# Optimization experiments

Measured on AMD Instinct MI355X. Metric: run time of the kernel, lower is better.

The kernel has to match this reference:

```python
import jax, jax.numpy as jnp
import numpy as np

NEG = -9e8

def _leaky(x):
    return jax.nn.leaky_relu(x, 0.01)

def _gru(x, h, wih, whh, bih, bhh):
    # torch.nn.GRUCell math
    gi = x @ wih.T + bih
    gh = h @ whh.T + bhh
    ir, iz, inn = jnp.split(gi, 3, axis=-1)
    hr, hz, hn = jnp.split(gh, 3, axis=-1)
    r = jax.nn.sigmoid(ir + hr)
    z = jax.nn.sigmoid(iz + hz)
    n = jnp.tanh(inn + r * hn)
    return (1.0 - z) * n + z * h

def _gather(feat, idx):
    # feat [B,S,F], idx [B,S,K] -> [B,S,K,F]; -1 wraps to last row, masked later (same as torch)
    return jax.vmap(lambda f, i: f[i])(feat, idx)

def setup_inputs() -> dict:
    key = jax.random.key(0)
    ks = jax.random.split(key, 32)
    B, S, K, F_in, E, R = 32, 512, 21, 26, 256, 3
    amino_list = jax.random.uniform(ks[0], (B, S, F_in), dtype=jnp.float32)
    idx = jax.random.randint(ks[1], (B, S, K), 0, S, dtype=jnp.int32)
    pad = jax.random.uniform(ks[2], (B, S, K)) < 0.3
    amino_degree_list = jnp.where(pad, jnp.int32(-1), idx)
    # variable sequence lengths for mask
    lens = jax.random.randint(ks[3], (B,), S // 2, S + 1)
    amino_mask = (jnp.arange(S)[None, :] < lens[:, None]).astype(jnp.float32)
    s = 0.05
    d = dict(
        amino_list=amino_list,
        amino_degree_list=amino_degree_list,
        amino_mask=amino_mask,
        emb_W=jax.random.normal(ks[4], (E, F_in)) * s,
        emb_b=jax.random.normal(ks[5], (E,)) * s,
        neigh_W=jax.random.normal(ks[6], (E, F_in)) * s,
        neigh_b=jax.random.normal(ks[7], (E,)) * s,
        align_W=jax.random.normal(ks[8], (R, 1, 2 * E)) * s,
        align_b=jax.random.normal(ks[9], (R, 1)) * s,
        attend_W=jax.random.normal(ks[10], (R, E, E)) * s,
        attend_b=jax.random.normal(ks[11], (R, E)) * s,
        gru_wih=jax.random.normal(ks[12], (R, 3 * E, E)) * s,
        gru_whh=jax.random.normal(ks[13], (R, 3 * E, E)) * s,
        gru_bih=jax.random.normal(ks[14], (R, 3 * E)) * s,
        gru_bhh=jax.random.normal(ks[15], (R, 3 * E)) * s,
        seq_align_W=jax.random.normal(ks[16], (1, 2 * E)) * s,
        seq_align_b=jax.random.normal(ks[17], (1,)) * s,
        seq_attend_W=jax.random.normal(ks[18], (E, E)) * s,
        seq_attend_b=jax.random.normal(ks[19], (E,)) * s,
        sgru_wih=jax.random.normal(ks[20], (3 * E, E)) * s,
        sgru_whh=jax.random.normal(ks[21], (3 * E, E)) * s,
        sgru_bih=jax.random.normal(ks[22], (3 * E,)) * s,
        sgru_bhh=jax.random.normal(ks[23], (3 * E,)) * s,
    )
    return d

RADIUS = 3
T_STEPS = 2

def reference(amino_list, amino_degree_list, amino_mask,
              emb_W, emb_b, neigh_W, neigh_b,
              align_W, align_b, attend_W, attend_b,
              gru_wih, gru_whh, gru_bih, gru_bhh,
              seq_align_W, seq_align_b, seq_attend_W, seq_attend_b,
              sgru_wih, sgru_whh, sgru_bih, sgru_bhh):
    B, S, _ = amino_list.shape
    E = emb_W.shape[0]
    K = amino_degree_list.shape[-1]

    mask3 = amino_mask[:, :, None]                       # [B,S,1]
    amino_feature = _leaky(amino_list @ emb_W.T + emb_b)  # [B,S,E]

    attend_mask = (amino_degree_list != -1).astype(jnp.float32)[..., None]   # [B,S,K,1]
    softmax_mask = jnp.where(amino_degree_list == -1, NEG, 0.0)[..., None]   # [B,S,K,1]

    # first radius step: neighbors from raw one-hot features via neighbor_fc
    neighbor = _gather(amino_list, amino_degree_list)                 # [B,S,K,F_in]
    neighbor_feature = _leaky(neighbor @ neigh_W.T + neigh_b)         # [B,S,K,E]

    h = amino_feature.reshape(B * S, E)
    activated = None
    for d in range(RADIUS):
        if d == 0:
            nbr = neighbor_feature
            cur = amino_feature
        else:
            nbr = _gather(activated, amino_degree_list)               # [B,S,K,E]
            cur = activated
        cur_exp = jnp.broadcast_to(cur[:, :, None, :], (B, S, K, E))
        feat_align = jnp.concatenate([cur_exp, nbr], axis=-1)         # [B,S,K,2E]
        score = _leaky(feat_align @ align_W[d].T + align_b[d]) + softmax_mask
        attw = jax.nn.softmax(score, axis=-2) * attend_mask           # [B,S,K,1]
        nbr_t = nbr @ attend_W[d].T + attend_b[d]                     # [B,S,K,E]
        context = jax.nn.elu(jnp.sum(attw * nbr_t, axis=-2))          # [B,S,E]
        h = _gru(context.reshape(B * S, E), h, gru_wih[d], gru_whh[d], gru_bih[d], gru_bhh[d])
        activated = jax.nn.relu(h.reshape(B, S, E))

    seq_feature = jnp.sum(activated * mask3, axis=-2)                 # [B,E]
    act_mol = jax.nn.relu(seq_feature)
    seq_softmax_mask = jnp.where(mask3 == 0.0, NEG, 0.0)              # [B,S,1]

    act_seq = act_mol
    for _ in range(T_STEPS):
        mol_exp = jnp.broadcast_to(act_mol[:, None, :], (B, S, E))
        sa = jnp.concatenate([mol_exp, activated], axis=-1)           # [B,S,2E]
        score = _leaky(sa @ seq_align_W.T + seq_align_b) + seq_softmax_mask
        w = jax.nn.softmax(score, axis=-2) * mask3                    # [B,S,1]
        feat_t = activated @ seq_attend_W.T + seq_attend_b            # [B,S,E]
        seq_context = jax.nn.elu(jnp.sum(w * feat_t, axis=-2))        # [B,E]
        seq_feature = _gru(seq_context, seq_feature, sgru_wih, sgru_whh, sgru_bih, sgru_bhh)
        act_seq = jax.nn.relu(seq_feature)
    return act_seq
```

## Files before the change

### kernel.cpp

```cpp
#include <hip/hip_runtime.h>
#include <hip/hip_bf16.h>
#include <math.h>


#define NEGC (-9.0e8f)

typedef __attribute__((ext_vector_type(8))) short bf16x8;
typedef __attribute__((ext_vector_type(4))) float f32x4;

__device__ __forceinline__ ushort f2bf(float x) {
    union { float f; unsigned u; } v; v.f = x;
    unsigned r = v.u + 0x7FFF + ((v.u >> 16) & 1);
    return (ushort)(r >> 16);
}
__device__ __forceinline__ float bf2f(ushort u) {
    union { unsigned u; float f; } v; v.u = ((unsigned)u) << 16;
    return v.f;
}
__device__ __forceinline__ float sigm_fast(float x) {
    return 1.f / (1.f + __expf(-x));
}
__device__ __forceinline__ float tanh_fast(float x) {
    return 1.f - 2.f / (__expf(2.f * x) + 1.f);
}
__device__ __forceinline__ float elu_fast(float x) {
    return x > 0.f ? x : (__expf(x) - 1.f);
}
__device__ __forceinline__ bf16x8 relu_bf8(bf16x8 v) {
    bf16x8 r;
#pragma unroll
    for (int i = 0; i < 8; ++i)
        r[i] = (v[i] & (short)0x8000) ? (short)0 : v[i];
    return r;
}

typedef const __attribute__((address_space(1))) void gvoid_t;
typedef __attribute__((address_space(3))) void lvoid_t;

__global__ __launch_bounds__(256) void cvt3_kernel(
    const float* __restrict__ s0, ushort* __restrict__ d0, int n0,
    const float* __restrict__ s1, ushort* __restrict__ d1, int n1,
    const float* __restrict__ s2, ushort* __restrict__ d2, int n2)
{
    int i = blockIdx.x * 256 + threadIdx.x;
    const float* s; ushort* dst; int l;
    if (i < n0) { s = s0; dst = d0; l = i; }
    else if (i < n0 + n1) { s = s1; dst = d1; l = i - n0; }
    else if (i < n0 + n1 + n2) { s = s2; dst = d2; l = i - n0 - n1; }
    else return;
    float4 v = *reinterpret_cast<const float4*>(s + (size_t)l * 4);
    ushort4 o; o.x = f2bf(v.x); o.y = f2bf(v.y); o.z = f2bf(v.z); o.w = f2bf(v.w);
    *reinterpret_cast<ushort4*>(dst + (size_t)l * 4) = o;
}

template<bool RELUA>
__global__ __launch_bounds__(256) void gemm_dual_kernel(
    const ushort* __restrict__ A0, const ushort* __restrict__ W0,
    const float* __restrict__ b0, ushort* __restrict__ C0, int n0t,
    int K,
    const float* __restrict__ dw1, const float* __restrict__ dw2,
    float* __restrict__ dout1, float* __restrict__ dout2)
{
    __shared__ __align__(16) short As[128 * 32];
    __shared__ __align__(16) short Bs[128 * 32];
    int nwg = gridDim.x;
    int q = nwg >> 3;
    int flat = blockIdx.x;
    int sw = (flat & 7) * q + (flat >> 3);
    int bmi = sw / n0t, bni = sw - bmi * n0t;
    const ushort* A = A0; const ushort* W = W0; const float* bias = b0;
    ushort* C = C0; int N = n0t << 7; int bn = bni << 7;
    int bm = bmi << 7;

    int tid = threadIdx.x;
    int lane = tid & 63;
    int w = tid >> 6;
    int wr = w >> 1, wc = w & 1;
    bool dots = (dout1 != nullptr) && (bni == 0);

    f32x4 acc[4][4];
#pragma unroll
    for (int m = 0; m < 4; ++m)
#pragma unroll
        for (int n = 0; n < 4; ++n) acc[m][n] = (f32x4){0.f, 0.f, 0.f, 0.f};
    float p1 = 0.f, p2 = 0.f;

    for (int k0 = 0; k0 < K; k0 += 32) {
#pragma unroll
        for (int i = 0; i < 2; ++i) {
            int e = w * 1024 + i * 512 + lane * 8;
            int r = e >> 5, c = e & 31;
            const ushort* ga = A + (size_t)(bm + r) * K + (k0 + c);
            const ushort* gw = W + (size_t)(bn + r) * K + (k0 + c);
            __builtin_amdgcn_global_load_lds((gvoid_t*)ga, (lvoid_t*)&As[w * 1024 + i * 512], 16, 0, 0);
            __builtin_amdgcn_global_load_lds((gvoid_t*)gw, (lvoid_t*)&Bs[w * 1024 + i * 512], 16, 0, 0);
        }
        __syncthreads();
        bf16x8 af[4], bw[4];
        int ra = wr * 64 + (lane & 15);
        int rb = wc * 64 + (lane & 15);
        int kc = (lane >> 4) * 8;
#pragma unroll
        for (int m = 0; m < 4; ++m) {
            af[m] = *reinterpret_cast<const bf16x8*>(&As[(ra + m * 16) * 32 + kc]);
            if (RELUA) af[m] = relu_bf8(af[m]);
        }
#pragma unroll
        for (int n = 0; n < 4; ++n)
            bw[n] = *reinterpret_cast<const bf16x8*>(&Bs[(rb + n * 16) * 32 + kc]);
#pragma unroll
        for (int m = 0; m < 4; ++m)
#pragma unroll
            for (int n = 0; n < 4; ++n)
                acc[m][n] = __builtin_amdgcn_mfma_f32_16x16x32_bf16(af[m], bw[n], acc[m][n], 0, 0, 0);
        if (dots) {
            int drow = tid >> 1, kh = (tid & 1) << 4;
            const short* ar = &As[drow * 32 + kh];
#pragma unroll
            for (int c = 0; c < 16; ++c) {
                float av = bf2f((ushort)ar[c]);
                if (RELUA) av = fmaxf(av, 0.f);
                p1 = fmaf(av, dw1[k0 + kh + c], p1);
                p2 = fmaf(av, dw2[k0 + kh + c], p2);
            }
        }
        __syncthreads();
    }

    if (dots) {
        p1 += __shfl_xor(p1, 1);
        p2 += __shfl_xor(p2, 1);
        if ((tid & 1) == 0) {
            dout1[bm + (tid >> 1)] = p1;
            dout2[bm + (tid >> 1)] = p2;
        }
    }

    int cr0 = bm + wr * 64 + ((lane >> 4) * 4);
    int cc0 = bn + wc * 64 + (lane & 15);
#pragma unroll
    for (int n = 0; n < 4; ++n) {
        int col = cc0 + n * 16;
        float bv = bias[col];
#pragma unroll
        for (int m = 0; m < 4; ++m) {
            int row0 = cr0 + m * 16;
#pragma unroll
            for (int j = 0; j < 4; ++j) {
                float v = acc[m][n][j] + bv;
                C[(size_t)(row0 + j) * N + col] = f2bf(v);
            }
        }
    }
}

template<bool TAIL>
__global__ __launch_bounds__(256) void gru_fused_kernel(
    const ushort* __restrict__ ctx, const ushort* __restrict__ wih,
    const float* __restrict__ bih, const ushort* __restrict__ whh,
    const float* __restrict__ bhh,
    const ushort* __restrict__ h_in, ushort* __restrict__ h_out,
    const float* __restrict__ mask, float* __restrict__ pool_part,
    const float* __restrict__ dsw, float* __restrict__ scor_part, int BS)
{
    __shared__ __align__(16) short lds[16384];
    int flat = blockIdx.x;
    int sw = (flat & 7) * 128 + (flat >> 3);
    int bmi = sw >> 2, ct = sw & 3;
    int bm = bmi << 6;
    int tid = threadIdx.x;
    int lane = tid & 63;
    int w = tid >> 6;
    int wr = w >> 1, wc = w & 1;

    f32x4 acc[6][2][2];
#pragma unroll
    for (int qq = 0; qq < 6; ++qq)
#pragma unroll
        for (int m = 0; m < 2; ++m)
#pragma unroll
            for (int n = 0; n < 2; ++n) acc[qq][m][n] = (f32x4){0.f, 0.f, 0.f, 0.f};

    int srow = tid >> 2, scol = (tid & 3) << 3;
    int ldst = (tid & 0xC0) * 8;
    for (int k0 = 0; k0 < 256; k0 += 32) {
        {
            const ushort* s0 = ctx  + (size_t)(bm + srow) * 256 + k0 + scol;
            const ushort* s1 = h_in + (size_t)(bm + srow) * 256 + k0 + scol;
            __builtin_amdgcn_global_load_lds((gvoid_t*)s0, (lvoid_t*)&lds[ldst], 16, 0, 0);
            __builtin_amdgcn_global_load_lds((gvoid_t*)s1, (lvoid_t*)&lds[2048 + ldst], 16, 0, 0);
#pragma unroll
            for (int qq = 0; qq < 6; ++qq) {
                const ushort* wb = (qq < 3) ? wih : whh;
                int slice = (qq < 3) ? qq : qq - 3;
                const ushort* sv = wb + (size_t)(slice * 256 + ct * 64 + srow) * 256 + k0 + scol;
                __builtin_amdgcn_global_load_lds((gvoid_t*)sv,
                    (lvoid_t*)&lds[(2 + qq) * 2048 + ldst], 16, 0, 0);
            }
        }
        __syncthreads();
        int rl = lane & 15;
        int kc = (lane >> 4) * 8;
        bf16x8 a_c[2], a_h[2];
#pragma unroll
        for (int m = 0; m < 2; ++m) {
            a_c[m] = *reinterpret_cast<const bf16x8*>(&lds[(wr * 32 + m * 16 + rl) * 32 + kc]);
            a_h[m] = *reinterpret_cast<const bf16x8*>(&lds[2048 + (wr * 32 + m * 16 + rl) * 32 + kc]);
        }
#pragma unroll
        for (int qq = 0; qq < 6; ++qq) {
            bf16x8 bw[2];
#pragma unroll
            for (int n = 0; n < 2; ++n)
                bw[n] = *reinterpret_cast<const bf16x8*>(
                    &lds[(2 + qq) * 2048 + (wc * 32 + n * 16 + rl) * 32 + kc]);
#pragma unroll
            for (int m = 0; m < 2; ++m)
#pragma unroll
                for (int n = 0; n < 2; ++n)
                    acc[qq][m][n] = __builtin_amdgcn_mfma_f32_16x16x32_bf16(
                        (qq < 3) ? a_c[m] : a_h[m], bw[n], acc[qq][m][n], 0, 0, 0);
        }
        __syncthreads();
    }

    int rl = lane & 15;
    int r0 = (lane >> 4) * 4;
    float mv[2][4];
    float dswv[2];
    if (TAIL) {
        int b_ = bm >> 9;
        int sbase = bm & 511;
#pragma unroll
        for (int m = 0; m < 2; ++m)
#pragma unroll
            for (int j = 0; j < 4; ++j)
                mv[m][j] = mask[b_ * 512 + sbase + wr * 32 + m * 16 + r0 + j];
#pragma unroll
        for (int n = 0; n < 2; ++n)
            dswv[n] = dsw[ct * 64 + wc * 32 + n * 16 + rl];
    }
    float pm[2] = {0.f, 0.f};
    float ps[2][4] = {{0.f, 0.f, 0.f, 0.f}, {0.f, 0.f, 0.f, 0.f}};

#pragma unroll
    for (int n = 0; n < 2; ++n) {
        int col = ct * 64 + wc * 32 + n * 16 + rl;
        float bir = bih[col], biz = bih[256 + col], bin = bih[512 + col];
        float bhr = bhh[col], bhz = bhh[256 + col], bhn = bhh[512 + col];
#pragma unroll
        for (int m = 0; m < 2; ++m) {
            int row0 = bm + wr * 32 + m * 16 + r0;
#pragma unroll
            for (int j = 0; j < 4; ++j) {
                size_t idx = (size_t)(row0 + j) * 256 + col;
                float r = sigm_fast(acc[0][m][n][j] + bir + acc[3][m][n][j] + bhr);
                float z = sigm_fast(acc[1][m][n][j] + biz + acc[4][m][n][j] + bhz);
                float nn = tanh_fast(acc[2][m][n][j] + bin + r * (acc[5][m][n][j] + bhn));
                float hold = bf2f(h_in[idx]);
                float hh = (1.f - z) * nn + z * hold;
                ushort hb = f2bf(hh);
                h_out[idx] = hb;
                if (TAIL) {
                    float a = fmaxf(bf2f(hb), 0.f);
                    pm[n] = fmaf(a, mv[m][j], pm[n]);
                    ps[m][j] = fmaf(a, dswv[n], ps[m][j]);
                }
            }
        }
    }

    if (TAIL) {
#pragma unroll
        for (int n = 0; n < 2; ++n) {
            float p = pm[n];
            p += __shfl_xor(p, 16);
            p += __shfl_xor(p, 32);
            if (lane < 16) {
                int b_ = bm >> 9;
                int sc = ((bm & 511) >> 5) + wr;
                int col = ct * 64 + wc * 32 + n * 16 + rl;
                pool_part[((size_t)b_ * 16 + sc) * 256 + col] = p;
            }
        }
#pragma unroll
        for (int m = 0; m < 2; ++m)
#pragma unroll
            for (int j = 0; j < 4; ++j) {
                float p = ps[m][j];
                p += __shfl_xor(p, 1);
                p += __shfl_xor(p, 2);
                p += __shfl_xor(p, 4);
                p += __shfl_xor(p, 8);
                if (rl == 0) {
                    int row = bm + wr * 32 + m * 16 + r0 + j;
                    scor_part[(size_t)(ct * 2 + wc) * BS + row] = p;
                }
            }
    }
}

__global__ __launch_bounds__(256) void embed_kernel(
    const float* __restrict__ amino, const float* __restrict__ embW,
    const float* __restrict__ embB, const float* __restrict__ neighW,
    const float* __restrict__ neighB, const float* __restrict__ alignW,
    ushort* __restrict__ h_bf, ushort* __restrict__ nf_bf,
    float* __restrict__ ca, float* __restrict__ cb)
{
    const int FIN = 26, FPAD = 28, ROWS = 64;
    __shared__ __align__(16) float xs[ROWS][FPAD];
    __shared__ float red1[ROWS][4];
    __shared__ float red2[ROWS][4];
    int tid = threadIdx.x;
    int lane = tid & 63, wv = tid >> 6;
    float wE[FPAD], wN[FPAD];
#pragma unroll
    for (int f = 0; f < FIN; ++f) {
        wE[f] = embW[tid * FIN + f];
        wN[f] = neighW[tid * FIN + f];
    }
    wE[26] = wE[27] = wN[26] = wN[27] = 0.f;
    float b1 = embB[tid], b2 = neighB[tid];
    float w1t = alignW[tid], w2t = alignW[256 + tid];
    int row0 = blockIdx.x * ROWS;
    for (int idx = tid; idx < ROWS * FPAD; idx += 256) {
        int r = idx / FPAD, f = idx - r * FPAD;
        xs[r][f] = (f < FIN) ? amino[(size_t)(row0 + r) * FIN + f] : 0.f;
    }
    __syncthreads();
    for (int r = 0; r < ROWS; ++r) {
        const float4* x4 = reinterpret_cast<const float4*>(xs[r]);
        float a = b1, c = b2;
#pragma unroll
        for (int q = 0; q < 7; ++q) {
            float4 x = x4[q];
            a = fmaf(x.x, wE[4 * q], a);     c = fmaf(x.x, wN[4 * q], c);
            a = fmaf(x.y, wE[4 * q + 1], a); c = fmaf(x.y, wN[4 * q + 1], c);
            a = fmaf(x.z, wE[4 * q + 2], a); c = fmaf(x.z, wN[4 * q + 2], c);
            a = fmaf(x.w, wE[4 * q + 3], a); c = fmaf(x.w, wN[4 * q + 3], c);
        }
        a = a > 0.f ? a : 0.01f * a;
        c = c > 0.f ? c : 0.01f * c;
        size_t idx = (size_t)(row0 + r) * 256 + tid;
        h_bf[idx] = f2bf(a);
        nf_bf[idx] = f2bf(c);
        float p1 = a * w1t, p2 = c * w2t;
#pragma unroll
        for (int off = 32; off > 0; off >>= 1) {
            p1 += __shfl_down(p1, off);
            p2 += __shfl_down(p2, off);
        }
        if (lane == 0) { red1[r][wv] = p1; red2[r][wv] = p2; }
    }
    __syncthreads();
    if (tid < ROWS)
        ca[row0 + tid] = red1[tid][0] + red1[tid][1] + red1[tid][2] + red1[tid][3];
    else if (tid < 2 * ROWS) {
        int r = tid - ROWS;
        cb[row0 + r] = red2[r][0] + red2[r][1] + red2[r][2] + red2[r][3];
    }
}

__global__ __launch_bounds__(256) void attn_kernel(
    const int* __restrict__ deg, const float* __restrict__ ca,
    const float* __restrict__ cbrow, const ushort* __restrict__ act_t,
    const float* __restrict__ alignB, int d,
    ushort* __restrict__ context_bf, int S)
{
    const int KNB = 21;
    int raw = blockIdx.x;
    int bid = (raw & 7) * 512 + (raw >> 3);
    int bs0 = bid * 4;
    int b = bs0 >> 9;
    int tid = threadIdx.x;
    int wv = tid >> 6, lane = tid & 63;
    int bs = bs0 + wv;
    __shared__ float ss[4][KNB];
    __shared__ int   sj[4][KNB];
    if (lane < KNB) {
        int j = deg[bs * KNB + lane];
        float cbv = (j >= 0) ? cbrow[b * S + j] : 0.f;
        float sc = ca[bs] + cbv + alignB[d];
        sc = sc > 0.f ? sc : 0.01f * sc;
        if (j < 0) sc += NEGC;
        sj[wv][lane] = j;
        ss[wv][lane] = sc;
    }
    __syncthreads();
    float mx = -3.4e38f;
#pragma unroll
    for (int k = 0; k < KNB; ++k) mx = fmaxf(mx, ss[wv][k]);
    float se[KNB];
    int js[KNB];
    float sum = 0.f;
#pragma unroll
    for (int k = 0; k < KNB; ++k) {
        int j = sj[wv][k];
        float e = __expf(ss[wv][k] - mx);
        sum += e;
        se[k] = (j >= 0) ? e : 0.f;
        js[k] = (j >= 0) ? j : 0;
    }
    float inv = 1.f / sum;
    const ushort* base = act_t + (size_t)b * S * 256 + lane * 4;
    float a0 = 0.f, a1 = 0.f, a2 = 0.f, a3 = 0.f;
#pragma unroll
    for (int k = 0; k < KNB; ++k) {
        ushort4 v = *reinterpret_cast<const ushort4*>(base + (size_t)js[k] * 256);
        float wk = se[k];
        a0 = fmaf(wk, bf2f(v.x), a0);
        a1 = fmaf(wk, bf2f(v.y), a1);
        a2 = fmaf(wk, bf2f(v.z), a2);
        a3 = fmaf(wk, bf2f(v.w), a3);
    }
    ushort4 o;
    o.x = f2bf(elu_fast(a0 * inv));
    o.y = f2bf(elu_fast(a1 * inv));
    o.z = f2bf(elu_fast(a2 * inv));
    o.w = f2bf(elu_fast(a3 * inv));
    *reinterpret_cast<ushort4*>(&context_bf[(size_t)bs * 256 + lane * 4]) = o;
}

__global__ __launch_bounds__(256) void seqpool_sm_kernel(
    const float* __restrict__ partial, const float* __restrict__ saW,
    const float* __restrict__ scor_part, const float* __restrict__ sab,
    const float* __restrict__ mask,
    float* __restrict__ seqfeat, float* __restrict__ wout,
    float* __restrict__ wsumb, int NC, int S, int BS)
{
    int b = blockIdx.x, tid = threadIdx.x;
    int lane = tid & 63, wv = tid >> 6;
    __shared__ float red[4];
    __shared__ float sw[512];
    __shared__ float r1[4], r2[4], r3[4];
    __shared__ float smd;
    float acc = 0.f;
    for (int c = 0; c < NC; ++c)
        acc += partial[((size_t)b * NC + c) * 256 + tid];
    seqfeat[b * 256 + tid] = acc;
    float am = fmaxf(acc, 0.f);
    float p = am * saW[tid];
#pragma unroll
    for (int off = 32; off > 0; off >>= 1) p += __shfl_down(p, off);
    if (lane == 0) red[wv] = p;
    __syncthreads();
    if (tid == 0) smd = red[0] + red[1] + red[2] + red[3];
    __syncthreads();
    float md = smd, sb = sab[0];
    float lm = -3.4e38f;
    for (int s = tid; s < S; s += 256) {
        int row = b * S + s;
        float praw = 0.f;
#pragma unroll
        for (int sl = 0; sl < 8; ++sl) praw += scor_part[(size_t)sl * BS + row];
        float sc = md + praw + sb;
        sc = sc > 0.f ? sc : 0.01f * sc;
        if (mask[row] == 0.f) sc += NEGC;
        sw[s] = sc;
        lm = fmaxf(lm, sc);
    }
#pragma unroll
    for (int off = 32; off > 0; off >>= 1) lm = fmaxf(lm, __shfl_down(lm, off));
    if (lane == 0) r1[wv] = lm;
    __syncthreads();
    float mx = fmaxf(fmaxf(r1[0], r1[1]), fmaxf(r1[2], r1[3]));
    float ls = 0.f, ms = 0.f;
    for (int s = tid; s < S; s += 256) {
        float e = __expf(sw[s] - mx);
        float em = e * mask[b * S + s];
        sw[s] = em;
        ls += e;
        ms += em;
    }
#pragma unroll
    for (int off = 32; off > 0; off >>= 1) {
        ls += __shfl_down(ls, off);
        ms += __shfl_down(ms, off);
    }
    if (lane == 0) { r2[wv] = ls; r3[wv] = ms; }
    __syncthreads();
    float inv = 1.f / (r2[0] + r2[1] + r2[2] + r2[3]);
    if (tid == 0) wsumb[b] = (r3[0] + r3[1] + r3[2] + r3[3]) * inv;
    for (int s = tid; s < S; s += 256)
        wout[b * S + s] = sw[s] * inv;
}

__global__ __launch_bounds__(256) void wpool_kernel(
    const float* __restrict__ w, const ushort* __restrict__ h,
    float* __restrict__ vpart, int S, int CH)
{
    int bc = blockIdx.x;
    int NC = S / CH;
    int b = bc / NC, c = bc - b * NC;
    int tid = threadIdx.x;
    int s0 = c * CH;
    const ushort* ab = h + ((size_t)b * S + s0) * 256;
    const float* wb = w + b * S + s0;
    float acc = 0.f;
    for (int s = 0; s < CH; ++s)
        acc = fmaf(wb[s], fmaxf(bf2f(ab[(size_t)s * 256 + tid]), 0.f), acc);
    vpart[(size_t)bc * 256 + tid] = acc;
}

__global__ __launch_bounds__(256) void sctx_mm_kernel(
    const float* __restrict__ vpart, const float* __restrict__ seqAttW,
    const float* __restrict__ seqAttB, const float* __restrict__ wsumb,
    float* __restrict__ sctx, int NC)
{
    int o = blockIdx.x * 4 + (threadIdx.x >> 6);
    int lane = threadIdx.x & 63;
    int b = o >> 8, col = o & 255;
    const float* wr_ = seqAttW + (size_t)col * 256;
    float p = 0.f;
#pragma unroll
    for (int i = 0; i < 4; ++i) {
        int idx = lane + 64 * i;
        float v = 0.f;
        for (int c = 0; c < 16; ++c)
            v += vpart[((size_t)b * 16 + c) * 256 + idx];
        p = fmaf(v, wr_[idx], p);
    }
#pragma unroll
    for (int off = 32; off > 0; off >>= 1) p += __shfl_down(p, off);
    if (lane == 0)
        sctx[o] = elu_fast(p + wsumb[b] * seqAttB[col]);
}

__global__ __launch_bounds__(256) void sgru_mm_kernel(
    const float* __restrict__ x, const float* __restrict__ hseq,
    const float* __restrict__ wih, const float* __restrict__ whh,
    const float* __restrict__ bih, const float* __restrict__ bhh,
    float* __restrict__ g, int full)
{
    int per_b = full ? 1536 : 768;
    int o = blockIdx.x * 4 + (threadIdx.x >> 6);
    int lane = threadIdx.x & 63;
    int b = o / per_b;
    int j = o - b * per_b;
    if (!full) j += 768;
    const float* src; const float* w; const float* bp; int jj;
    if (j < 768) { src = x + b * 256; w = wih; bp = bih; jj = j; }
    else         { src = hseq + b * 256; w = whh; bp = bhh; jj = j - 768; }
    float p = 0.f;
#pragma unroll
    for (int i = 0; i < 4; ++i) {
        int idx = lane + 64 * i;
        p = fmaf(src[idx], w[(size_t)jj * 256 + idx], p);
    }
#pragma unroll
    for (int off = 32; off > 0; off >>= 1) p += __shfl_down(p, off);
    if (lane == 0) g[b * 1536 + j] = p + bp[jj];
}

__global__ __launch_bounds__(256) void sgru_gate_kernel(
    const float* __restrict__ g, float* __restrict__ hseq, float* __restrict__ out)
{
    int b = blockIdx.x, e = threadIdx.x;
    const float* gr = g + b * 1536;
    float r = sigm_fast(gr[e] + gr[768 + e]);
    float z = sigm_fast(gr[256 + e] + gr[1024 + e]);
    float n = tanh_fast(gr[512 + e] + r * gr[1280 + e]);
    float hv = hseq[b * 256 + e];
    float hn = (1.f - z) * n + z * hv;
    hseq[b * 256 + e] = hn;
    out[b * 256 + e] = fmaxf(hn, 0.f);
}

extern "C" void kernel_launch(void* const* d_in, const int* in_sizes, int n_in,
                              void* d_out, int out_size, void* d_ws, size_t ws_size,
                              hipStream_t stream)
{
    const float* amino   = (const float*)d_in[0];
    const int*   deg     = (const int*)  d_in[1];
    const float* mask    = (const float*)d_in[2];
    const float* embW    = (const float*)d_in[3];
    const float* embB    = (const float*)d_in[4];
    const float* neighW  = (const float*)d_in[5];
    const float* neighB  = (const float*)d_in[6];
    const float* alignW  = (const float*)d_in[7];
    const float* alignB  = (const float*)d_in[8];
    const float* attendW = (const float*)d_in[9];
    const float* attendB = (const float*)d_in[10];
    const float* gruWih  = (const float*)d_in[11];
    const float* gruWhh  = (const float*)d_in[12];
    const float* gruBih  = (const float*)d_in[13];
    const float* gruBhh  = (const float*)d_in[14];
    const float* saW     = (const float*)d_in[15];
    const float* saB     = (const float*)d_in[16];
    const float* seqAttW = (const float*)d_in[17];
    const float* seqAttB = (const float*)d_in[18];
    const float* sWih    = (const float*)d_in[19];
    const float* sWhh    = (const float*)d_in[20];
    const float* sBih    = (const float*)d_in[21];
    const float* sBhh    = (const float*)d_in[22];
    float* out = (float*)d_out;

    const int B = 32, S = 512;
    const int BS = B * S;
    const size_t N1 = (size_t)BS * 256;

    ushort* hA     = (ushort*)d_ws;
    ushort* hB     = hA + N1;
    ushort* nb_bf  = hB + N1;
    ushort* att_bf = nb_bf + N1;
    ushort* attW_bf = att_bf + N1;
    ushort* wih_bf  = attW_bf + 3 * 256 * 256;
    ushort* whh_bf  = wih_bf + 3 * 768 * 256;
    float* smalls = (float*)(whh_bf + 3 * 768 * 256);
    float* ca    = smalls;
    float* cb    = ca + BS;
    float* wbuf  = cb + BS;
    float* scorp = wbuf + BS;
    float* seqf  = scorp + 8 * BS;
    float* sctx  = seqf + B * 256;
    float* wsumb = sctx + B * 256;
    float* g     = wsumb + 256;
    float* part  = g + B * 1536;
    float* vpart = part + B * 16 * 256;

    const int c0 = (3 * 256 * 256) / 4, c1 = (3 * 768 * 256) / 4,
              c2 = (3 * 768 * 256) / 4;
    cvt3_kernel<<<(c0 + c1 + c2 + 255) / 256, 256, 0, stream>>>(
        attendW, attW_bf, c0, gruWih, wih_bf, c1, gruWhh, whh_bf, c2);

    embed_kernel<<<BS / 64, 256, 0, stream>>>(amino, embW, embB, neighW, neighB, alignW,
                                              hA, nb_bf, ca, cb);

    for (int d = 0; d < 3; ++d) {
        const ushort* h_in  = (d & 1) ? hB : hA;
        ushort*       h_out = (d & 1) ? hA : hB;
        if (d == 0) {
            gemm_dual_kernel<false><<<128 * 2, 256, 0, stream>>>(
                nb_bf, attW_bf, attendB, att_bf, 2, 256,
                (const float*)nullptr, (const float*)nullptr,
                (float*)nullptr, (float*)nullptr);
        } else {
            gemm_dual_kernel<true><<<128 * 2, 256, 0, stream>>>(
                h_in, attW_bf + d * 256 * 256, attendB + d * 256, att_bf, 2, 256,
                alignW + d * 512, alignW + d * 512 + 256, ca, cb);
        }
        attn_kernel<<<BS / 4, 256, 0, stream>>>(deg, ca, cb, att_bf, alignB, d, nb_bf, S);
        if (d < 2) {
            gru_fused_kernel<false><<<1024, 256, 0, stream>>>(
                nb_bf, wih_bf + d * 768 * 256, gruBih + d * 768,
                whh_bf + d * 768 * 256, gruBhh + d * 768, h_in, h_out,
                (const float*)nullptr, (float*)nullptr,
                (const float*)nullptr, (float*)nullptr, BS);
        } else {
            gru_fused_kernel<true><<<1024, 256, 0, stream>>>(
                nb_bf, wih_bf + d * 768 * 256, gruBih + d * 768,
                whh_bf + d * 768 * 256, gruBhh + d * 768, h_in, h_out,
                mask, part, saW + 256, scorp, BS);
        }
    }

    seqpool_sm_kernel<<<B, 256, 0, stream>>>(part, saW, scorp, saB, mask,
                                             seqf, wbuf, wsumb, 16, S, BS);
    wpool_kernel<<<B * 16, 256, 0, stream>>>(wbuf, hB, vpart, S, 32);
    sctx_mm_kernel<<<B * 256 / 4, 256, 0, stream>>>(vpart, seqAttW, seqAttB, wsumb, sctx, 16);

    sgru_mm_kernel<<<B * 1536 / 4, 256, 0, stream>>>(sctx, seqf, sWih, sWhh, sBih, sBhh, g, 1);
    sgru_gate_kernel<<<B, 256, 0, stream>>>(g, seqf, out);
    sgru_mm_kernel<<<B * 768 / 4, 256, 0, stream>>>(sctx, seqf, sWih, sWhh, sBih, sBhh, g, 0);
    sgru_gate_kernel<<<B, 256, 0, stream>>>(g, seqf, out);
}
```

Measured before the change: 245.7 us.

## Merge weight conversion with embedding and fuse sequence GRU tail into one kernel

The bf16 weight-conversion kernel and the embedding kernel become a single launch, with the block index choosing which role each block plays. The tail chain (weighted pooling, seq-attend matvec, two GRU matvec launches and two gate launches) is replaced by one per-batch kernel that keeps intermediates in shared memory and reuses the input-side GRU projection across both steps. This removes about seven launches and the global round-trips between them. In exchange, the tail runs on only 32 blocks, each pooling over all 512 sequence positions serially, so that work is spread over far fewer blocks than before.

```diff
diff --git a/kernel.cpp b/kernel.cpp
--- a/kernel.cpp
+++ b/kernel.cpp
@@ -37,20 +37,81 @@
 typedef const __attribute__((address_space(1))) void gvoid_t;
 typedef __attribute__((address_space(3))) void lvoid_t;
 
-__global__ __launch_bounds__(256) void cvt3_kernel(
+__global__ __launch_bounds__(256) void cvt_embed_kernel(
     const float* __restrict__ s0, ushort* __restrict__ d0, int n0,
     const float* __restrict__ s1, ushort* __restrict__ d1, int n1,
-    const float* __restrict__ s2, ushort* __restrict__ d2, int n2)
+    const float* __restrict__ s2, ushort* __restrict__ d2, int n2,
+    int cvtb,
+    const float* __restrict__ amino, const float* __restrict__ embW,
+    const float* __restrict__ embB, const float* __restrict__ neighW,
+    const float* __restrict__ neighB, const float* __restrict__ alignW,
+    ushort* __restrict__ h_bf, ushort* __restrict__ nf_bf,
+    float* __restrict__ ca, float* __restrict__ cb)
 {
-    int i = blockIdx.x * 256 + threadIdx.x;
-    const float* s; ushort* dst; int l;
-    if (i < n0) { s = s0; dst = d0; l = i; }
-    else if (i < n0 + n1) { s = s1; dst = d1; l = i - n0; }
-    else if (i < n0 + n1 + n2) { s = s2; dst = d2; l = i - n0 - n1; }
-    else return;
-    float4 v = *reinterpret_cast<const float4*>(s + (size_t)l * 4);
-    ushort4 o; o.x = f2bf(v.x); o.y = f2bf(v.y); o.z = f2bf(v.z); o.w = f2bf(v.w);
-    *reinterpret_cast<ushort4*>(dst + (size_t)l * 4) = o;
+    if ((int)blockIdx.x < cvtb) {
+        int i = blockIdx.x * 256 + threadIdx.x;
+        const float* s; ushort* dst; int l;
+        if (i < n0) { s = s0; dst = d0; l = i; }
+        else if (i < n0 + n1) { s = s1; dst = d1; l = i - n0; }
+        else if (i < n0 + n1 + n2) { s = s2; dst = d2; l = i - n0 - n1; }
+        else return;
+        float4 v = *reinterpret_cast<const float4*>(s + (size_t)l * 4);
+        ushort4 o; o.x = f2bf(v.x); o.y = f2bf(v.y); o.z = f2bf(v.z); o.w = f2bf(v.w);
+        *reinterpret_cast<ushort4*>(dst + (size_t)l * 4) = o;
+        return;
+    }
+    const int FIN = 26, FPAD = 28, ROWS = 64;
+    __shared__ __align__(16) float xs[ROWS][FPAD];
+    __shared__ float red1[ROWS][4];
+    __shared__ float red2[ROWS][4];
+    int tid = threadIdx.x;
+    int lane = tid & 63, wv = tid >> 6;
+    float wE[FPAD], wN[FPAD];
+#pragma unroll
+    for (int f = 0; f < FIN; ++f) {
+        wE[f] = embW[tid * FIN + f];
+        wN[f] = neighW[tid * FIN + f];
+    }
+    wE[26] = wE[27] = wN[26] = wN[27] = 0.f;
+    float b1 = embB[tid], b2 = neighB[tid];
+    float w1t = alignW[tid], w2t = alignW[256 + tid];
+    int row0 = (blockIdx.x - cvtb) * ROWS;
+    for (int idx = tid; idx < ROWS * FPAD; idx += 256) {
+        int r = idx / FPAD, f = idx - r * FPAD;
+        xs[r][f] = (f < FIN) ? amino[(size_t)(row0 + r) * FIN + f] : 0.f;
+    }
+    __syncthreads();
+    for (int r = 0; r < ROWS; ++r) {
+        const float4* x4 = reinterpret_cast<const float4*>(xs[r]);
+        float a = b1, c = b2;
+#pragma unroll
+        for (int q = 0; q < 7; ++q) {
+            float4 x = x4[q];
+            a = fmaf(x.x, wE[4 * q], a);     c = fmaf(x.x, wN[4 * q], c);
+            a = fmaf(x.y, wE[4 * q + 1], a); c = fmaf(x.y, wN[4 * q + 1], c);
+            a = fmaf(x.z, wE[4 * q + 2], a); c = fmaf(x.z, wN[4 * q + 2], c);
+            a = fmaf(x.w, wE[4 * q + 3], a); c = fmaf(x.w, wN[4 * q + 3], c);
+        }
+        a = a > 0.f ? a : 0.01f * a;
+        c = c > 0.f ? c : 0.01f * c;
+        size_t idx = (size_t)(row0 + r) * 256 + tid;
+        h_bf[idx] = f2bf(a);
+        nf_bf[idx] = f2bf(c);
+        float p1 = a * w1t, p2 = c * w2t;
+#pragma unroll
+        for (int off = 32; off > 0; off >>= 1) {
+            p1 += __shfl_down(p1, off);
+            p2 += __shfl_down(p2, off);
+        }
+        if (lane == 0) { red1[r][wv] = p1; red2[r][wv] = p2; }
+    }
+    __syncthreads();
+    if (tid < ROWS)
+        ca[row0 + tid] = red1[tid][0] + red1[tid][1] + red1[tid][2] + red1[tid][3];
+    else if (tid < 2 * ROWS) {
+        int r = tid - ROWS;
+        cb[row0 + r] = red2[r][0] + red2[r][1] + red2[r][2] + red2[r][3];
+    }
 }
 
 template<bool RELUA>
@@ -297,67 +358,6 @@
                     scor_part[(size_t)(ct * 2 + wc) * BS + row] = p;
                 }
             }
-    }
-}
-
-__global__ __launch_bounds__(256) void embed_kernel(
-    const float* __restrict__ amino, const float* __restrict__ embW,
-    const float* __restrict__ embB, const float* __restrict__ neighW,
-    const float* __restrict__ neighB, const float* __restrict__ alignW,
-    ushort* __restrict__ h_bf, ushort* __restrict__ nf_bf,
-    float* __restrict__ ca, float* __restrict__ cb)
-{
-    const int FIN = 26, FPAD = 28, ROWS = 64;
-    __shared__ __align__(16) float xs[ROWS][FPAD];
-    __shared__ float red1[ROWS][4];
-    __shared__ float red2[ROWS][4];
-    int tid = threadIdx.x;
-    int lane = tid & 63, wv = tid >> 6;
-    float wE[FPAD], wN[FPAD];
-#pragma unroll
-    for (int f = 0; f < FIN; ++f) {
-        wE[f] = embW[tid * FIN + f];
-        wN[f] = neighW[tid * FIN + f];
-    }
-    wE[26] = wE[27] = wN[26] = wN[27] = 0.f;
-    float b1 = embB[tid], b2 = neighB[tid];
-    float w1t = alignW[tid], w2t = alignW[256 + tid];
-    int row0 = blockIdx.x * ROWS;
-    for (int idx = tid; idx < ROWS * FPAD; idx += 256) {
-        int r = idx / FPAD, f = idx - r * FPAD;
-        xs[r][f] = (f < FIN) ? amino[(size_t)(row0 + r) * FIN + f] : 0.f;
-    }
-    __syncthreads();
-    for (int r = 0; r < ROWS; ++r) {
-        const float4* x4 = reinterpret_cast<const float4*>(xs[r]);
-        float a = b1, c = b2;
-#pragma unroll
-        for (int q = 0; q < 7; ++q) {
-            float4 x = x4[q];
-            a = fmaf(x.x, wE[4 * q], a);     c = fmaf(x.x, wN[4 * q], c);
-            a = fmaf(x.y, wE[4 * q + 1], a); c = fmaf(x.y, wN[4 * q + 1], c);
-            a = fmaf(x.z, wE[4 * q + 2], a); c = fmaf(x.z, wN[4 * q + 2], c);
-            a = fmaf(x.w, wE[4 * q + 3], a); c = fmaf(x.w, wN[4 * q + 3], c);
-        }
-        a = a > 0.f ? a : 0.01f * a;
-        c = c > 0.f ? c : 0.01f * c;
-        size_t idx = (size_t)(row0 + r) * 256 + tid;
-        h_bf[idx] = f2bf(a);
-        nf_bf[idx] = f2bf(c);
-        float p1 = a * w1t, p2 = c * w2t;
-#pragma unroll
-        for (int off = 32; off > 0; off >>= 1) {
-            p1 += __shfl_down(p1, off);
-            p2 += __shfl_down(p2, off);
-        }
-        if (lane == 0) { red1[r][wv] = p1; red2[r][wv] = p2; }
-    }
-    __syncthreads();
-    if (tid < ROWS)
-        ca[row0 + tid] = red1[tid][0] + red1[tid][1] + red1[tid][2] + red1[tid][3];
-    else if (tid < 2 * ROWS) {
-        int r = tid - ROWS;
-        cb[row0 + r] = red2[r][0] + red2[r][1] + red2[r][2] + red2[r][3];
     }
 }
 
@@ -485,85 +485,78 @@
         wout[b * S + s] = sw[s] * inv;
 }
 
-__global__ __launch_bounds__(256) void wpool_kernel(
-    const float* __restrict__ w, const ushort* __restrict__ h,
-    float* __restrict__ vpart, int S, int CH)
+__global__ __launch_bounds__(256) void sgru_tail_kernel(
+    const float* __restrict__ wbuf, const ushort* __restrict__ h,
+    const float* __restrict__ seqAttW, const float* __restrict__ seqAttB,
+    const float* __restrict__ wsumb, const float* __restrict__ seqf,
+    const float* __restrict__ sWih, const float* __restrict__ sWhh,
+    const float* __restrict__ sBih, const float* __restrict__ sBhh,
+    float* __restrict__ out, int S)
 {
-    int bc = blockIdx.x;
-    int NC = S / CH;
-    int b = bc / NC, c = bc - b * NC;
-    int tid = threadIdx.x;
-    int s0 = c * CH;
-    const ushort* ab = h + ((size_t)b * S + s0) * 256;
-    const float* wb = w + b * S + s0;
+    __shared__ float V[256];
+    __shared__ float x[256];
+    __shared__ float hs[256];
+    __shared__ float giL[768];
+    __shared__ float ghL[768];
+    int b = blockIdx.x, tid = threadIdx.x;
+    int lane = tid & 63, wv = tid >> 6;
+
     float acc = 0.f;
-    for (int s = 0; s < CH; ++s)
-        acc = fmaf(wb[s], fmaxf(bf2f(ab[(size_t)s * 256 + tid]), 0.f), acc);
-    vpart[(size_t)bc * 256 + tid] = acc;
-}
-
-__global__ __launch_bounds__(256) void sctx_mm_kernel(
-    const float* __restrict__ vpart, const float* __restrict__ seqAttW,
-    const float* __restrict__ seqAttB, const float* __restrict__ wsumb,
-    float* __restrict__ sctx, int NC)
-{
-    int o = blockIdx.x * 4 + (threadIdx.x >> 6);
-    int lane = threadIdx.x & 63;
-    int b = o >> 8, col = o & 255;
-    const float* wr_ = seqAttW + (size_t)col * 256;
-    float p = 0.f;
-#pragma unroll
-    for (int i = 0; i < 4; ++i) {
-        int idx = lane + 64 * i;
-        float v = 0.f;
-        for (int c = 0; c < 16; ++c)
-            v += vpart[((size_t)b * 16 + c) * 256 + idx];
-        p = fmaf(v, wr_[idx], p);
-    }
-#pragma unroll
-    for (int off = 32; off > 0; off >>= 1) p += __shfl_down(p, off);
-    if (lane == 0)
-        sctx[o] = elu_fast(p + wsumb[b] * seqAttB[col]);
-}
-
-__global__ __launch_bounds__(256) void sgru_mm_kernel(
-    const float* __restrict__ x, const float* __restrict__ hseq,
-    const float* __restrict__ wih, const float* __restrict__ whh,
-    const float* __restrict__ bih, const float* __restrict__ bhh,
-    float* __restrict__ g, int full)
-{
-    int per_b = full ? 1536 : 768;
-    int o = blockIdx.x * 4 + (threadIdx.x >> 6);
-    int lane = threadIdx.x & 63;
-    int b = o / per_b;
-    int j = o - b * per_b;
-    if (!full) j += 768;
-    const float* src; const float* w; const float* bp; int jj;
-    if (j < 768) { src = x + b * 256; w = wih; bp = bih; jj = j; }
-    else         { src = hseq + b * 256; w = whh; bp = bhh; jj = j - 768; }
-    float p = 0.f;
-#pragma unroll
-    for (int i = 0; i < 4; ++i) {
-        int idx = lane + 64 * i;
-        p = fmaf(src[idx], w[(size_t)jj * 256 + idx], p);
-    }
-#pragma unroll
-    for (int off = 32; off > 0; off >>= 1) p += __shfl_down(p, off);
-    if (lane == 0) g[b * 1536 + j] = p + bp[jj];
-}
-
-__global__ __launch_bounds__(256) void sgru_gate_kernel(
-    const float* __restrict__ g, float* __restrict__ hseq, float* __restrict__ out)
-{
-    int b = blockIdx.x, e = threadIdx.x;
-    const float* gr = g + b * 1536;
-    float r = sigm_fast(gr[e] + gr[768 + e]);
-    float z = sigm_fast(gr[256 + e] + gr[1024 + e]);
-    float n = tanh_fast(gr[512 + e] + r * gr[1280 + e]);
-    float hv = hseq[b * 256 + e];
-    float hn = (1.f - z) * n + z * hv;
-    hseq[b * 256 + e] = hn;
-    out[b * 256 + e] = fmaxf(hn, 0.f);
+    const ushort* hb = h + (size_t)b * S * 256;
+    const float* wb = wbuf + b * S;
+    for (int s = 0; s < S; ++s)
+        acc = fmaf(wb[s], fmaxf(bf2f(hb[(size_t)s * 256 + tid]), 0.f), acc);
+    V[tid] = acc;
+    hs[tid] = seqf[b * 256 + tid];
+    __syncthreads();
+
+    float wsb = wsumb[b];
+    for (int col = wv * 64; col < wv * 64 + 64; ++col) {
+        const float* wr_ = seqAttW + (size_t)col * 256;
+        float p = 0.f;
+#pragma unroll
+        for (int i = 0; i < 4; ++i)
+            p = fmaf(V[lane + 64 * i], wr_[lane + 64 * i], p);
+#pragma unroll
+        for (int off = 32; off > 0; off >>= 1) p += __shfl_down(p, off);
+        if (lane == 0) x[col] = elu_fast(p + wsb * seqAttB[col]);
+    }
+    __syncthreads();
+
+    for (int j = wv; j < 768; j += 4) {
+        const float* wr_ = sWih + (size_t)j * 256;
+        float p = 0.f;
+#pragma unroll
+        for (int i = 0; i < 4; ++i)
+            p = fmaf(x[lane + 64 * i], wr_[lane + 64 * i], p);
+#pragma unroll
+        for (int off = 32; off > 0; off >>= 1) p += __shfl_down(p, off);
+        if (lane == 0) giL[j] = p + sBih[j];
+    }
+    __syncthreads();
+
+    float hn = 0.f;
+    for (int t = 0; t < 2; ++t) {
+        for (int j = wv; j < 768; j += 4) {
+            const float* wr_ = sWhh + (size_t)j * 256;
+            float p = 0.f;
+#pragma unroll
+            for (int i = 0; i < 4; ++i)
+                p = fmaf(hs[lane + 64 * i], wr_[lane + 64 * i], p);
+#pragma unroll
+            for (int off = 32; off > 0; off >>= 1) p += __shfl_down(p, off);
+            if (lane == 0) ghL[j] = p + sBhh[j];
+        }
+        __syncthreads();
+        float r = sigm_fast(giL[tid] + ghL[tid]);
+        float z = sigm_fast(giL[256 + tid] + ghL[256 + tid]);
+        float n = tanh_fast(giL[512 + tid] + r * ghL[512 + tid]);
+        hn = (1.f - z) * n + z * hs[tid];
+        __syncthreads();
+        hs[tid] = hn;
+        __syncthreads();
+    }
+    out[b * 256 + tid] = fmaxf(hn, 0.f);
 }
 
 extern "C" void kernel_launch(void* const* d_in, const int* in_sizes, int n_in,
@@ -612,19 +605,15 @@
     float* wbuf  = cb + BS;
     float* scorp = wbuf + BS;
     float* seqf  = scorp + 8 * BS;
-    float* sctx  = seqf + B * 256;
-    float* wsumb = sctx + B * 256;
-    float* g     = wsumb + 256;
-    float* part  = g + B * 1536;
-    float* vpart = part + B * 16 * 256;
+    float* wsumb = seqf + B * 256;
+    float* part  = wsumb + 256;
 
     const int c0 = (3 * 256 * 256) / 4, c1 = (3 * 768 * 256) / 4,
               c2 = (3 * 768 * 256) / 4;
-    cvt3_kernel<<<(c0 + c1 + c2 + 255) / 256, 256, 0, stream>>>(
-        attendW, attW_bf, c0, gruWih, wih_bf, c1, gruWhh, whh_bf, c2);
-
-    embed_kernel<<<BS / 64, 256, 0, stream>>>(amino, embW, embB, neighW, neighB, alignW,
-                                              hA, nb_bf, ca, cb);
+    const int cvtb = (c0 + c1 + c2 + 255) / 256;
+    cvt_embed_kernel<<<cvtb + BS / 64, 256, 0, stream>>>(
+        attendW, attW_bf, c0, gruWih, wih_bf, c1, gruWhh, whh_bf, c2, cvtb,
+        amino, embW, embB, neighW, neighB, alignW, hA, nb_bf, ca, cb);
 
     for (int d = 0; d < 3; ++d) {
         const ushort* h_in  = (d & 1) ? hB : hA;
@@ -656,11 +645,6 @@
 
     seqpool_sm_kernel<<<B, 256, 0, stream>>>(part, saW, scorp, saB, mask,
                                              seqf, wbuf, wsumb, 16, S, BS);
-    wpool_kernel<<<B * 16, 256, 0, stream>>>(wbuf, hB, vpart, S, 32);
-    sctx_mm_kernel<<<B * 256 / 4, 256, 0, stream>>>(vpart, seqAttW, seqAttB, wsumb, sctx, 16);
-
-    sgru_mm_kernel<<<B * 1536 / 4, 256, 0, stream>>>(sctx, seqf, sWih, sWhh, sBih, sBhh, g, 1);
-    sgru_gate_kernel<<<B, 256, 0, stream>>>(g, seqf, out);
-    sgru_mm_kernel<<<B * 768 / 4, 256, 0, stream>>>(sctx, seqf, sWih, sWhh, sBih, sBhh, g, 0);
-    sgru_gate_kernel<<<B, 256, 0, stream>>>(g, seqf, out);
-}
+    sgru_tail_kernel<<<B, 256, 0, stream>>>(wbuf, hB, seqAttW, seqAttB, wsumb, seqf,
+                                            sWih, sWhh, sBih, sBhh, out, S);
+}
```

Measured after the change: 647.3 us. 2.63x slower.
